# Kernel tuning notes

Hardware: AMD Instinct MI355X
Metric: run time of the kernel (lower is better)

The kernel has to match this reference:

```python
import jax, jax.numpy as jnp
import numpy as np

N, E, K, IN, OUT = 20000, 320000, 5, 256, 128
NAN_FRAC = 0.3


def setup_inputs() -> dict:
    key = jax.random.key(0)
    ks = jax.random.split(key, 8)
    x = jax.random.normal(ks[0], (N, IN), dtype=jnp.float32)
    nan_mask = jax.random.uniform(ks[1], (N, IN)) < NAN_FRAC
    x = jnp.where(nan_mask, jnp.nan, x)  # missing features as NaN
    edge_index = jax.random.randint(ks[2], (2, E), 0, N, dtype=jnp.int64)
    logp = jax.nn.log_softmax(jax.random.normal(ks[3], (K,), dtype=jnp.float32))
    means = jax.random.normal(ks[4], (K, IN), dtype=jnp.float32)
    logvars = jax.random.normal(ks[5], (K, IN), dtype=jnp.float32) * 0.1
    xav = 1.414 * np.sqrt(6.0 / (IN + OUT))
    weight = jax.random.uniform(ks[6], (IN, OUT), dtype=jnp.float32, minval=-xav, maxval=xav)
    bias = jnp.zeros((OUT,), dtype=jnp.float32)
    return {"x": x, "edge_index": edge_index, "logp": logp, "means": means,
            "logvars": logvars, "weight": weight, "bias": bias}


def _ex_relu(mu, sigma):
    # E[relu(X)] for X ~ N(mu, sigma); sigma is the variance
    sigma_s = jnp.where(sigma == 0, 1e-10, sigma)
    ss = jnp.sqrt(sigma_s)
    w = mu / ss
    nr = ss * (jnp.exp(-0.5 * w * w) / np.sqrt(2 * np.pi)
               + 0.5 * w * (1.0 + jax.lax.erf(w / np.sqrt(2))))
    return jnp.where(sigma == 0, jnp.maximum(mu, 0.0), nr)


def _gcn_norm(edge_index, num_nodes):
    # add self-loops, symmetric D^-1/2 A D^-1/2 normalization
    row = jnp.concatenate([edge_index[0], jnp.arange(num_nodes, dtype=edge_index.dtype)])
    col = jnp.concatenate([edge_index[1], jnp.arange(num_nodes, dtype=edge_index.dtype)])
    ones = jnp.ones(row.shape[0], dtype=jnp.float32)
    deg = jax.ops.segment_sum(ones, row, num_segments=num_nodes)
    dinv = jnp.where(deg > 0, jax.lax.rsqrt(deg), 0.0)
    wn = dinv[row] * dinv[col]
    return row, col, wn


def reference(x, edge_index, logp, means, logvars, weight, bias):
    n = x.shape[0]
    dim = x.shape[1]
    row, col, wn = _gcn_norm(edge_index, n)
    wn2 = wn * wn  # adj2 = adj * adj (elementwise on sparse values)

    isnan = jnp.isnan(x)                                       # [N, IN]
    variances = jnp.exp(logvars)                               # [K, IN]
    mean_mat = jnp.where(isnan[None], means[:, None, :], x[None])      # [K, N, IN]
    var_mat = jnp.where(isnan[None], variances[:, None, :], 0.0)       # [K, N, IN]

    transform_x = jnp.einsum('kni,io->kno', mean_mat, weight) + bias   # [K, N, OUT]
    transform_covs = jnp.einsum('kni,io->kno', var_mat, weight * weight)

    def spmm(vals, X):  # segment-sum SpMM: out[r] += vals_e * X[c]
        return jax.ops.segment_sum(X[col] * vals[:, None], row, num_segments=n)

    conv_x = jax.vmap(lambda X: spmm(wn, X))(transform_x)      # [K, N, OUT]
    conv_covs = jax.vmap(lambda X: spmm(wn2, X))(transform_covs)

    expected_x = _ex_relu(conv_x, conv_covs)                   # [K, N, OUT]

    # GMM responsibilities per node
    log_n = (-0.5 * jnp.sum((mean_mat - means[:, None, :]) ** 2 / variances[:, None, :], axis=2)
             - 0.5 * dim * np.log(2 * np.pi) - 0.5 * jnp.sum(logvars))  # [K, N]
    gamma = jax.nn.softmax(logp[:, None] + log_n, axis=0)      # [K, N]

    return jnp.sum(expected_x * gamma[:, :, None], axis=0)     # [N, OUT]
```

## Files before the change

kernel.cpp:

```cpp
#include <hip/hip_runtime.h>
#include <stdint.h>

#define N_NODES 20000
#define N_EDGES 320000
#define K_MIX 5
#define IN_F 256
#define OUT_F 128
#define NT 11
#define TC (NT * OUT_F)

typedef __attribute__((ext_vector_type(8))) short short8;
typedef __attribute__((ext_vector_type(4))) float floatx4;

__device__ __forceinline__ float bf2f(unsigned int u) {
  union { unsigned int i; float f; } v;
  v.i = (u & 0xffffu) << 16;
  return v.f;
}
__device__ __forceinline__ unsigned short f2bf(float f) {
  union { float f; unsigned int i; } v;
  v.f = f;
  unsigned int x = v.i;
  unsigned int r = (x + 0x7fffu + ((x >> 16) & 1u)) >> 16;
  return (unsigned short)r;
}

__device__ __forceinline__ float exrelu(float mu, float sig) {
  if (sig < 1e-30f) return fmaxf(mu, 0.f);
  float ss = sqrtf(sig);
  float w = mu / ss;
  float e = __expf(-0.5f * w * w);
  float axv = fabsf(w) * 0.70710678118654752f;
  float t = 1.f / (1.f + 0.3275911f * axv);
  float poly = t * (0.254829592f +
              t * (-0.284496736f +
              t * (1.421413741f +
              t * (-1.453152027f + t * 1.061405429f))));
  float erfv = 1.f - poly * e;
  erfv = copysignf(erfv, w);
  return ss * (e * 0.3989422804014327f + 0.5f * w * (1.f + erfv));
}

__global__ void k_deg(const int* __restrict__ row, int* __restrict__ deg) {
  int t = blockIdx.x * 256 + threadIdx.x;
  if (t < N_EDGES) atomicAdd(&deg[row[t]], 1);
}

__global__ void k_scan1(const int* __restrict__ deg, int* __restrict__ startofs,
                        int* __restrict__ bsums, float* __restrict__ dinv) {
  __shared__ int sd[256];
  int t = threadIdx.x;
  int i = blockIdx.x * 256 + t;
  int v = (i < N_NODES) ? deg[i] : 0;
  if (i < N_NODES) dinv[i] = rsqrtf((float)(v + 1));
  sd[t] = v;
  __syncthreads();
  for (int off = 1; off < 256; off <<= 1) {
    int u = (t >= off) ? sd[t - off] : 0;
    __syncthreads();
    sd[t] += u;
    __syncthreads();
  }
  if (i < N_NODES) startofs[i] = sd[t] - v;
  if (t == 255) bsums[blockIdx.x] = sd[255];
}

__global__ void k_scan2(int* __restrict__ bsums, int nb) {
  __shared__ int sd[128];
  int t = threadIdx.x;
  int v = (t < nb) ? bsums[t] : 0;
  sd[t] = v;
  __syncthreads();
  for (int off = 1; off < 128; off <<= 1) {
    int u = (t >= off) ? sd[t - off] : 0;
    __syncthreads();
    sd[t] += u;
    __syncthreads();
  }
  if (t < nb) bsums[t] = sd[t] - v;
}

__global__ void k_scan3(int* __restrict__ startofs, int* __restrict__ cursor,
                        const int* __restrict__ bsums) {
  int i = blockIdx.x * 256 + threadIdx.x;
  if (i < N_NODES) {
    int s0 = startofs[i] + bsums[blockIdx.x];
    startofs[i] = s0;
    cursor[i] = s0;
  }
}

__global__ void k_scatter(const int* __restrict__ row, const int* __restrict__ col,
                          const float* __restrict__ dinv, int* __restrict__ cursor,
                          int* __restrict__ csr_col, float* __restrict__ csr_w) {
  int t = blockIdx.x * 256 + threadIdx.x;
  if (t < N_EDGES) {
    int r = row[t], c = col[t];
    int p = atomicAdd(&cursor[r], 1);
    csr_col[p] = c;
    csr_w[p] = dinv[r] * dinv[c];
  }
}

__global__ void k_buildB(const float* __restrict__ W, const float* __restrict__ means,
                         const float* __restrict__ logvars, unsigned short* __restrict__ Bt) {
  int idx = blockIdx.x * 256 + threadIdx.x;
  int j = idx >> 15;
  int rem = idx & 32767;
  int n = rem >> 8;
  int kk = rem & 255;
  float wv = W[kk * OUT_F + n];
  float val;
  if (j == 0) val = wv;
  else if (j <= 5) val = means[(j - 1) * IN_F + kk] * wv;
  else val = expf(logvars[(j - 6) * IN_F + kk]) * wv * wv;
  Bt[idx] = f2bf(val);
}

__global__ void k_prepx(const float* __restrict__ x, const float* __restrict__ logp,
                        const float* __restrict__ means, const float* __restrict__ logvars,
                        unsigned short* __restrict__ X0, float* __restrict__ gamma) {
  __shared__ float s_mean[K_MIX * IN_F];
  __shared__ float s_rv[K_MIX * IN_F];
  int t = threadIdx.x;
  for (int j = t; j < K_MIX * IN_F; j += 256) {
    s_mean[j] = means[j];
    s_rv[j] = expf(-logvars[j]);
  }
  __syncthreads();
  int node = blockIdx.x * 4 + (t >> 6);
  if (node >= N_NODES) return;
  int lane = t & 63;
  float4 xv = *(const float4*)(x + (size_t)node * IN_F + 4 * lane);
  float xf[4] = {xv.x, xv.y, xv.z, xv.w};
  float gsum[K_MIX] = {0, 0, 0, 0, 0};
  ushort4 o;
  unsigned short* op = (unsigned short*)&o;
#pragma unroll
  for (int j = 0; j < 4; j++) {
    bool nn = (xf[j] != xf[j]);
    op[j] = nn ? (unsigned short)0x7FC0 : f2bf(xf[j]);
    if (!nn) {
      int fi = 4 * lane + j;
#pragma unroll
      for (int k = 0; k < K_MIX; k++) {
        float d = xf[j] - s_mean[k * IN_F + fi];
        gsum[k] += d * d * s_rv[k * IN_F + fi];
      }
    }
  }
  *(ushort4*)(X0 + node * IN_F + 4 * lane) = o;
#pragma unroll
  for (int k = 0; k < K_MIX; k++)
    for (int off = 32; off; off >>= 1) gsum[k] += __shfl_xor(gsum[k], off, 64);
  if (lane == 0) {
    float lg[K_MIX], mx = -1e30f;
#pragma unroll
    for (int k = 0; k < K_MIX; k++) {
      lg[k] = logp[k] - 0.5f * gsum[k];
      mx = fmaxf(mx, lg[k]);
    }
    float se = 0.f;
#pragma unroll
    for (int k = 0; k < K_MIX; k++) { lg[k] = expf(lg[k] - mx); se += lg[k]; }
    float inv = 1.f / se;
#pragma unroll
    for (int k = 0; k < K_MIX; k++) gamma[node * K_MIX + k] = lg[k] * inv;
  }
}

__global__ __launch_bounds__(64) void k_spmm(const unsigned short* __restrict__ X0,
                       const int* __restrict__ startofs, const int* __restrict__ deg,
                       const float* __restrict__ dinv, const int* __restrict__ csr_col,
                       const float* __restrict__ csr_w, unsigned short* __restrict__ G,
                       float* __restrict__ sArr) {
  int node = blockIdx.x;
  int lane = threadIdx.x;
  int fo = 4 * lane;
  float ax[4] = {0, 0, 0, 0}, am[4] = {0, 0, 0, 0}, am2[4] = {0, 0, 0, 0};
  float ssum = 0.f;
  float ws = dinv[node];
  ws = ws * ws;
  int st = startofs[node];
  int total = deg[node] + 1;
  ushort4 zero4 = {0, 0, 0, 0};
  ushort4 B0 = zero4, B1 = zero4, B2 = zero4, B3 = zero4,
          B4 = zero4, B5 = zero4, B6 = zero4, B7 = zero4;
  float W0 = 0.f, W1 = 0.f, W2 = 0.f, W3 = 0.f,
        W4 = 0.f, W5 = 0.f, W6 = 0.f, W7 = 0.f;
  B0 = *(const ushort4*)(X0 + node * IN_F + fo); W0 = ws;
#define PFILL(S)                                                      \
  if (S < total) {                                                    \
    int c = csr_col[st + (S - 1)];                                    \
    W##S = csr_w[st + (S - 1)];                                       \
    B##S = *(const ushort4*)(X0 + c * IN_F + fo);                     \
  }
  PFILL(1) PFILL(2) PFILL(3) PFILL(4) PFILL(5) PFILL(6) PFILL(7)
#undef PFILL

#define STEP(S)                                                       \
  if (W##S != 0.f) {                                                  \
    float wv = W##S, wv2 = wv * wv;                                   \
    ssum += wv;                                                       \
    const unsigned short* xp = (const unsigned short*)&B##S;          \
    _Pragma("unroll")                                                 \
    for (int j = 0; j < 4; j++) {                                     \
      float xf = bf2f(xp[j]);                                         \
      bool nn = (xf != xf);                                           \
      ax[j] = fmaf(wv, nn ? 0.f : xf, ax[j]);                         \
      am[j] += nn ? wv : 0.f;                                         \
      am2[j] += nn ? wv2 : 0.f;                                       \
    }                                                                 \
  }                                                                   \
  if (base + 8 + S < total) {                                         \
    int c = csr_col[st + base + 7 + S];                               \
    W##S = csr_w[st + base + 7 + S];                                  \
    B##S = *(const ushort4*)(X0 + c * IN_F + fo);                     \
  } else {                                                            \
    W##S = 0.f;                                                       \
  }

  for (int base = 0; base < total; base += 8) {
    STEP(0) STEP(1) STEP(2) STEP(3) STEP(4) STEP(5) STEP(6) STEP(7)
  }
#undef STEP

  ushort4 o;
  o.x = f2bf(ax[0]); o.y = f2bf(ax[1]); o.z = f2bf(ax[2]); o.w = f2bf(ax[3]);
  *(ushort4*)(G + node * 768 + fo) = o;
  o.x = f2bf(am[0]); o.y = f2bf(am[1]); o.z = f2bf(am[2]); o.w = f2bf(am[3]);
  *(ushort4*)(G + node * 768 + 256 + fo) = o;
  o.x = f2bf(am2[0]); o.y = f2bf(am2[1]); o.z = f2bf(am2[2]); o.w = f2bf(am2[3]);
  *(ushort4*)(G + node * 768 + 512 + fo) = o;
  if (lane == 0) sArr[node] = ssum;
}

__global__ __launch_bounds__(256) void k_gemm(const unsigned short* __restrict__ G,
                                              const unsigned short* __restrict__ Bt,
                                              unsigned short* __restrict__ T) {
  __shared__ char Als[128 * 64 * 2];
  __shared__ char Bls[128 * 64 * 2];
  int mt = blockIdx.x, jt = blockIdx.y;
  int aoff = (jt == 0) ? 0 : (jt <= 5 ? 256 : 512);
  int t = threadIdx.x, wave = t >> 6, lane = t & 63;
  int wr = wave >> 1, wc = wave & 1;
  int quad = lane >> 4, l16 = lane & 15;
  const unsigned short* Bp = Bt + (size_t)jt * 32768;

  floatx4 acc[4][4];
  floatx4 z = {0.f, 0.f, 0.f, 0.f};
#pragma unroll
  for (int mi = 0; mi < 4; mi++)
#pragma unroll
    for (int ni = 0; ni < 4; ni++) acc[mi][ni] = z;

  for (int k0 = 0; k0 < 256; k0 += 64) {
    __syncthreads();
#pragma unroll
    for (int i = 0; i < 4; i++) {
      int f = i * 256 + t;
      int r = f >> 3, cchunk = f & 7;
      int sw = cchunk ^ (r & 7);
      int gr = mt * 128 + r;
      if (gr >= N_NODES) gr = N_NODES - 1;
      *(uint4*)(Als + r * 128 + sw * 16) =
          *(const uint4*)(G + (size_t)gr * 768 + aoff + k0 + cchunk * 8);
      *(uint4*)(Bls + r * 128 + sw * 16) =
          *(const uint4*)(Bp + (size_t)r * 256 + k0 + cchunk * 8);
    }
    __syncthreads();
#pragma unroll
    for (int ks = 0; ks < 2; ks++) {
      int cc = ks * 4 + quad;
      short8 a[4], b[4];
#pragma unroll
      for (int mi = 0; mi < 4; mi++) {
        int r = wr * 64 + mi * 16 + l16;
        a[mi] = *(const short8*)(Als + r * 128 + (cc ^ (r & 7)) * 16);
      }
#pragma unroll
      for (int ni = 0; ni < 4; ni++) {
        int r = wc * 64 + ni * 16 + l16;
        b[ni] = *(const short8*)(Bls + r * 128 + (cc ^ (r & 7)) * 16);
      }
#pragma unroll
      for (int mi = 0; mi < 4; mi++)
#pragma unroll
        for (int ni = 0; ni < 4; ni++)
          acc[mi][ni] = __builtin_amdgcn_mfma_f32_16x16x32_bf16(a[mi], b[ni], acc[mi][ni], 0, 0, 0);
    }
  }
#pragma unroll
  for (int mi = 0; mi < 4; mi++)
#pragma unroll
    for (int ni = 0; ni < 4; ni++) {
      int gc = jt * 128 + wc * 64 + ni * 16 + l16;
#pragma unroll
      for (int reg = 0; reg < 4; reg++) {
        int gr = mt * 128 + wr * 64 + mi * 16 + quad * 4 + reg;
        if (gr < N_NODES) T[(size_t)gr * TC + gc] = f2bf(acc[mi][ni][reg]);
      }
    }
}

__global__ void k_final(const unsigned short* __restrict__ T, const float* __restrict__ gamma,
                        const float* __restrict__ sArr, const float* __restrict__ bias,
                        float* __restrict__ out) {
  int t = threadIdx.x;
  int node = blockIdx.x * 4 + (t >> 6);
  if (node >= N_NODES) return;
  int lane = t & 63;
  int o0 = 2 * lane;
  float g[K_MIX];
#pragma unroll
  for (int k = 0; k < K_MIX; k++) g[k] = gamma[node * K_MIX + k];
  float sv = sArr[node];
  float b0 = bias[o0], b1 = bias[o0 + 1];
  const unsigned short* Tr = T + (size_t)node * TC;
  unsigned int c0u = *(const unsigned int*)(Tr + o0);
  float cx0 = bf2f(c0u), cx1 = bf2f(c0u >> 16);
  float a0 = 0.f, a1 = 0.f;
#pragma unroll
  for (int k = 0; k < K_MIX; k++) {
    unsigned int tm = *(const unsigned int*)(Tr + 128 * (1 + k) + o0);
    unsigned int tv = *(const unsigned int*)(Tr + 128 * (6 + k) + o0);
    float mu0 = cx0 + bf2f(tm) + b0 * sv;
    float mu1 = cx1 + bf2f(tm >> 16) + b1 * sv;
    a0 += g[k] * exrelu(mu0, bf2f(tv));
    a1 += g[k] * exrelu(mu1, bf2f(tv >> 16));
  }
  float2 ov = {a0, a1};
  *(float2*)(out + (size_t)node * OUT_F + o0) = ov;
}

extern "C" void kernel_launch(void* const* d_in, const int* in_sizes, int n_in,
                              void* d_out, int out_size, void* d_ws, size_t ws_size,
                              hipStream_t stream) {
  const float* x = (const float*)d_in[0];
  const int* ei = (const int*)d_in[1];
  const float* logp = (const float*)d_in[2];
  const float* means = (const float*)d_in[3];
  const float* lvar = (const float*)d_in[4];
  const float* W = (const float*)d_in[5];
  const float* bias = (const float*)d_in[6];
  float* out = (float*)d_out;
  const int* row = ei;
  const int* col = ei + N_EDGES;

  char* p = (char*)d_ws;
  auto alloc = [&](size_t bytes) -> char* {
    char* q = p;
    p += (bytes + 255) & ~((size_t)255);
    return q;
  };
  int* deg = (int*)alloc(N_NODES * 4);
  float* dinv = (float*)alloc(N_NODES * 4);
  int* startofs = (int*)alloc(N_NODES * 4);
  int* cursor = (int*)alloc(N_NODES * 4);
  int* bsums = (int*)alloc(128 * 4);
  int* csr_col = (int*)alloc((size_t)N_EDGES * 4);
  float* csr_w = (float*)alloc((size_t)N_EDGES * 4);
  float* gamma = (float*)alloc((size_t)N_NODES * K_MIX * 4);
  float* sArr = (float*)alloc(N_NODES * 4);
  unsigned short* Bt = (unsigned short*)alloc((size_t)NT * 128 * 256 * 2);
  unsigned short* X0 = (unsigned short*)alloc((size_t)N_NODES * IN_F * 2);
  unsigned short* G = (unsigned short*)alloc((size_t)N_NODES * 768 * 2);
  unsigned short* T = (unsigned short*)alloc((size_t)N_NODES * TC * 2);

  hipMemsetAsync(deg, 0, N_NODES * 4, stream);
  k_deg<<<(N_EDGES + 255) / 256, 256, 0, stream>>>(row, deg);
  k_scan1<<<79, 256, 0, stream>>>(deg, startofs, bsums, dinv);
  k_scan2<<<1, 128, 0, stream>>>(bsums, 79);
  k_scan3<<<79, 256, 0, stream>>>(startofs, cursor, bsums);
  k_scatter<<<(N_EDGES + 255) / 256, 256, 0, stream>>>(row, col, dinv, cursor, csr_col, csr_w);
  k_buildB<<<(NT * 128 * 256) / 256, 256, 0, stream>>>(W, means, lvar, Bt);
  k_prepx<<<N_NODES / 4, 256, 0, stream>>>(x, logp, means, lvar, X0, gamma);
  k_spmm<<<N_NODES, 64, 0, stream>>>(X0, startofs, deg, dinv, csr_col, csr_w, G, sArr);
  k_gemm<<<dim3((N_NODES + 127) / 128, NT), 256, 0, stream>>>(G, Bt, T);
  k_final<<<N_NODES / 4, 256, 0, stream>>>(T, gamma, sArr, bias, out);
}
```

Baseline: 226.7 us.

## Fuse GEMM with ExReLU/gamma epilogue and drop intermediate T buffer

Replaces the separate GEMM kernel, which wrote an 11-column-tile bf16 intermediate T, and the final epilogue kernel with one kernel. Each block holds a 64-row tile of G fully in LDS and loops over the mixture components, computing mean and variance accumulators and applying exrelu with gamma weighting in registers. This removes the write and re-read of the large intermediate and one launch. In exchange it uses smaller 64x64 tiles, loop-carried accumulators and heavier LDS use, which may lower MFMA efficiency and occupancy. Intermediate rounding to bf16 is also removed.

```diff
diff --git a/kernel.cpp b/kernel.cpp
--- a/kernel.cpp
+++ b/kernel.cpp
@@ -7,7 +7,6 @@
 #define IN_F 256
 #define OUT_F 128
 #define NT 11
-#define TC (NT * OUT_F)
 
 typedef __attribute__((ext_vector_type(8))) short short8;
 typedef __attribute__((ext_vector_type(4))) float floatx4;
@@ -235,102 +234,164 @@
   if (lane == 0) sArr[node] = ssum;
 }
 
-__global__ __launch_bounds__(256) void k_gemm(const unsigned short* __restrict__ G,
-                                              const unsigned short* __restrict__ Bt,
-                                              unsigned short* __restrict__ T) {
-  __shared__ char Als[128 * 64 * 2];
-  __shared__ char Bls[128 * 64 * 2];
-  int mt = blockIdx.x, jt = blockIdx.y;
-  int aoff = (jt == 0) ? 0 : (jt <= 5 ? 256 : 512);
+__global__ __launch_bounds__(256, 2) void k_gemm_ep(
+    const unsigned short* __restrict__ G, const unsigned short* __restrict__ Bt,
+    const float* __restrict__ gamma, const float* __restrict__ sArr,
+    const float* __restrict__ bias, float* __restrict__ out) {
+  __shared__ __align__(16) char A1ls[64 * 512];
+  __shared__ __align__(16) char A2ls[64 * 512];
+  __shared__ __align__(16) char Bls0[64 * 128];
+  __shared__ __align__(16) char Bls1[64 * 128];
+  int mt = blockIdx.x, ch = blockIdx.y;
   int t = threadIdx.x, wave = t >> 6, lane = t & 63;
   int wr = wave >> 1, wc = wave & 1;
   int quad = lane >> 4, l16 = lane & 15;
-  const unsigned short* Bp = Bt + (size_t)jt * 32768;
-
-  floatx4 acc[4][4];
+
   floatx4 z = {0.f, 0.f, 0.f, 0.f};
-#pragma unroll
-  for (int mi = 0; mi < 4; mi++)
-#pragma unroll
-    for (int ni = 0; ni < 4; ni++) acc[mi][ni] = z;
-
+  floatx4 cx[2][2], oa[2][2];
+#pragma unroll
+  for (int mi = 0; mi < 2; mi++)
+#pragma unroll
+    for (int ni = 0; ni < 2; ni++) { cx[mi][ni] = z; oa[mi][ni] = z; }
+
+#define STAGE_A(dst, aoff_)                                              \
+  {                                                                      \
+    _Pragma("unroll")                                                    \
+    for (int i = 0; i < 8; i++) {                                        \
+      int f = i * 256 + t;                                               \
+      int r = f >> 5, c = f & 31;                                        \
+      int sw = c ^ (r & 7);                                              \
+      int gr = mt * 64 + r;                                              \
+      if (gr >= N_NODES) gr = N_NODES - 1;                               \
+      *(uint4*)((dst) + r * 512 + sw * 16) =                             \
+          *(const uint4*)(G + (size_t)gr * 768 + (aoff_) + c * 8);       \
+    }                                                                    \
+  }
+
+#define STAGE_B(dst, jt_, k0_)                                           \
+  {                                                                      \
+    _Pragma("unroll")                                                    \
+    for (int i = 0; i < 2; i++) {                                        \
+      int f = i * 256 + t;                                               \
+      int r = f >> 3, c = f & 7;                                         \
+      int sw = c ^ (r & 7);                                              \
+      *(uint4*)((dst) + r * 128 + sw * 16) =                             \
+          *(const uint4*)(Bt + (size_t)(jt_)*32768 +                     \
+                          (ch * 64 + r) * 256 + (k0_) + c * 8);          \
+    }                                                                    \
+  }
+
+  STAGE_A(A1ls, 0)
   for (int k0 = 0; k0 < 256; k0 += 64) {
     __syncthreads();
-#pragma unroll
-    for (int i = 0; i < 4; i++) {
-      int f = i * 256 + t;
-      int r = f >> 3, cchunk = f & 7;
-      int sw = cchunk ^ (r & 7);
-      int gr = mt * 128 + r;
+    STAGE_B(Bls0, 0, k0)
+    __syncthreads();
+#pragma unroll
+    for (int ks = 0; ks < 2; ks++) {
+      int ccA = (k0 >> 3) + ks * 4 + quad;
+      int ccB = ks * 4 + quad;
+      short8 a[2], b[2];
+#pragma unroll
+      for (int mi = 0; mi < 2; mi++) {
+        int r = wr * 32 + mi * 16 + l16;
+        a[mi] = *(const short8*)(A1ls + r * 512 + (ccA ^ (r & 7)) * 16);
+      }
+#pragma unroll
+      for (int ni = 0; ni < 2; ni++) {
+        int r = wc * 32 + ni * 16 + l16;
+        b[ni] = *(const short8*)(Bls0 + r * 128 + (ccB ^ (r & 7)) * 16);
+      }
+#pragma unroll
+      for (int mi = 0; mi < 2; mi++)
+#pragma unroll
+        for (int ni = 0; ni < 2; ni++)
+          cx[mi][ni] = __builtin_amdgcn_mfma_f32_16x16x32_bf16(a[mi], b[ni], cx[mi][ni], 0, 0, 0);
+    }
+  }
+
+  __syncthreads();
+  STAGE_A(A1ls, 256)
+  STAGE_A(A2ls, 512)
+
+  int gr0 = mt * 64 + wr * 32 + quad * 4;
+  int gc0 = ch * 64 + wc * 32 + l16;
+  float svr[2][4];
+#pragma unroll
+  for (int mi = 0; mi < 2; mi++)
+#pragma unroll
+    for (int reg = 0; reg < 4; reg++) {
+      int gr = gr0 + mi * 16 + reg;
       if (gr >= N_NODES) gr = N_NODES - 1;
-      *(uint4*)(Als + r * 128 + sw * 16) =
-          *(const uint4*)(G + (size_t)gr * 768 + aoff + k0 + cchunk * 8);
-      *(uint4*)(Bls + r * 128 + sw * 16) =
-          *(const uint4*)(Bp + (size_t)r * 256 + k0 + cchunk * 8);
+      svr[mi][reg] = sArr[gr];
     }
-    __syncthreads();
-#pragma unroll
-    for (int ks = 0; ks < 2; ks++) {
-      int cc = ks * 4 + quad;
-      short8 a[4], b[4];
-#pragma unroll
-      for (int mi = 0; mi < 4; mi++) {
-        int r = wr * 64 + mi * 16 + l16;
-        a[mi] = *(const short8*)(Als + r * 128 + (cc ^ (r & 7)) * 16);
-      }
-#pragma unroll
-      for (int ni = 0; ni < 4; ni++) {
-        int r = wc * 64 + ni * 16 + l16;
-        b[ni] = *(const short8*)(Bls + r * 128 + (cc ^ (r & 7)) * 16);
-      }
-#pragma unroll
-      for (int mi = 0; mi < 4; mi++)
-#pragma unroll
-        for (int ni = 0; ni < 4; ni++)
-          acc[mi][ni] = __builtin_amdgcn_mfma_f32_16x16x32_bf16(a[mi], b[ni], acc[mi][ni], 0, 0, 0);
+  float biasr[2] = {bias[gc0], bias[gc0 + 16]};
+
+#pragma unroll 1
+  for (int k = 0; k < K_MIX; k++) {
+    floatx4 tm[2][2], tv[2][2];
+#pragma unroll
+    for (int mi = 0; mi < 2; mi++)
+#pragma unroll
+      for (int ni = 0; ni < 2; ni++) { tm[mi][ni] = z; tv[mi][ni] = z; }
+    for (int k0 = 0; k0 < 256; k0 += 64) {
+      __syncthreads();
+      STAGE_B(Bls0, 1 + k, k0)
+      STAGE_B(Bls1, 6 + k, k0)
+      __syncthreads();
+#pragma unroll
+      for (int ks = 0; ks < 2; ks++) {
+        int ccA = (k0 >> 3) + ks * 4 + quad;
+        int ccB = ks * 4 + quad;
+        short8 a1[2], a2[2], bm[2], bv[2];
+#pragma unroll
+        for (int mi = 0; mi < 2; mi++) {
+          int r = wr * 32 + mi * 16 + l16;
+          int sa = r * 512 + (ccA ^ (r & 7)) * 16;
+          a1[mi] = *(const short8*)(A1ls + sa);
+          a2[mi] = *(const short8*)(A2ls + sa);
+        }
+#pragma unroll
+        for (int ni = 0; ni < 2; ni++) {
+          int r = wc * 32 + ni * 16 + l16;
+          int sb = r * 128 + (ccB ^ (r & 7)) * 16;
+          bm[ni] = *(const short8*)(Bls0 + sb);
+          bv[ni] = *(const short8*)(Bls1 + sb);
+        }
+#pragma unroll
+        for (int mi = 0; mi < 2; mi++)
+#pragma unroll
+          for (int ni = 0; ni < 2; ni++) {
+            tm[mi][ni] = __builtin_amdgcn_mfma_f32_16x16x32_bf16(a1[mi], bm[ni], tm[mi][ni], 0, 0, 0);
+            tv[mi][ni] = __builtin_amdgcn_mfma_f32_16x16x32_bf16(a2[mi], bv[ni], tv[mi][ni], 0, 0, 0);
+          }
+      }
     }
-  }
-#pragma unroll
-  for (int mi = 0; mi < 4; mi++)
-#pragma unroll
-    for (int ni = 0; ni < 4; ni++) {
-      int gc = jt * 128 + wc * 64 + ni * 16 + l16;
+#pragma unroll
+    for (int mi = 0; mi < 2; mi++)
 #pragma unroll
       for (int reg = 0; reg < 4; reg++) {
-        int gr = mt * 128 + wr * 64 + mi * 16 + quad * 4 + reg;
-        if (gr < N_NODES) T[(size_t)gr * TC + gc] = f2bf(acc[mi][ni][reg]);
-      }
-    }
-}
-
-__global__ void k_final(const unsigned short* __restrict__ T, const float* __restrict__ gamma,
-                        const float* __restrict__ sArr, const float* __restrict__ bias,
-                        float* __restrict__ out) {
-  int t = threadIdx.x;
-  int node = blockIdx.x * 4 + (t >> 6);
-  if (node >= N_NODES) return;
-  int lane = t & 63;
-  int o0 = 2 * lane;
-  float g[K_MIX];
-#pragma unroll
-  for (int k = 0; k < K_MIX; k++) g[k] = gamma[node * K_MIX + k];
-  float sv = sArr[node];
-  float b0 = bias[o0], b1 = bias[o0 + 1];
-  const unsigned short* Tr = T + (size_t)node * TC;
-  unsigned int c0u = *(const unsigned int*)(Tr + o0);
-  float cx0 = bf2f(c0u), cx1 = bf2f(c0u >> 16);
-  float a0 = 0.f, a1 = 0.f;
-#pragma unroll
-  for (int k = 0; k < K_MIX; k++) {
-    unsigned int tm = *(const unsigned int*)(Tr + 128 * (1 + k) + o0);
-    unsigned int tv = *(const unsigned int*)(Tr + 128 * (6 + k) + o0);
-    float mu0 = cx0 + bf2f(tm) + b0 * sv;
-    float mu1 = cx1 + bf2f(tm >> 16) + b1 * sv;
-    a0 += g[k] * exrelu(mu0, bf2f(tv));
-    a1 += g[k] * exrelu(mu1, bf2f(tv >> 16));
-  }
-  float2 ov = {a0, a1};
-  *(float2*)(out + (size_t)node * OUT_F + o0) = ov;
+        int gr = gr0 + mi * 16 + reg;
+        if (gr >= N_NODES) gr = N_NODES - 1;
+        float g = gamma[gr * K_MIX + k];
+#pragma unroll
+        for (int ni = 0; ni < 2; ni++) {
+          float mu = cx[mi][ni][reg] + tm[mi][ni][reg] + biasr[ni] * svr[mi][reg];
+          oa[mi][ni][reg] += g * exrelu(mu, tv[mi][ni][reg]);
+        }
+      }
+  }
+
+#pragma unroll
+  for (int mi = 0; mi < 2; mi++)
+#pragma unroll
+    for (int ni = 0; ni < 2; ni++)
+#pragma unroll
+      for (int reg = 0; reg < 4; reg++) {
+        int gr = gr0 + mi * 16 + reg;
+        if (gr < N_NODES) out[(size_t)gr * OUT_F + gc0 + ni * 16] = oa[mi][ni][reg];
+      }
+#undef STAGE_A
+#undef STAGE_B
 }
 
 extern "C" void kernel_launch(void* const* d_in, const int* in_sizes, int n_in,
@@ -365,7 +426,6 @@
   unsigned short* Bt = (unsigned short*)alloc((size_t)NT * 128 * 256 * 2);
   unsigned short* X0 = (unsigned short*)alloc((size_t)N_NODES * IN_F * 2);
   unsigned short* G = (unsigned short*)alloc((size_t)N_NODES * 768 * 2);
-  unsigned short* T = (unsigned short*)alloc((size_t)N_NODES * TC * 2);
 
   hipMemsetAsync(deg, 0, N_NODES * 4, stream);
   k_deg<<<(N_EDGES + 255) / 256, 256, 0, stream>>>(row, deg);
@@ -376,6 +436,5 @@
   k_buildB<<<(NT * 128 * 256) / 256, 256, 0, stream>>>(W, means, lvar, Bt);
   k_prepx<<<N_NODES / 4, 256, 0, stream>>>(x, logp, means, lvar, X0, gamma);
   k_spmm<<<N_NODES, 64, 0, stream>>>(X0, startofs, deg, dinv, csr_col, csr_w, G, sArr);
-  k_gemm<<<dim3((N_NODES + 127) / 128, NT), 256, 0, stream>>>(G, Bt, T);
-  k_final<<<N_NODES / 4, 256, 0, stream>>>(T, gamma, sArr, bias, out);
-}
+  k_gemm_ep<<<dim3((N_NODES + 63) / 64, 2), 256, 0, stream>>>(G, Bt, gamma, sArr, bias, out);
+}
```

After: 242.2 us. +6.9%, slower.
